# Optimization experiments

Hardware: AMD Instinct MI355X
Metric: run time of the kernel (lower is better)

## Reference

```python
import jax, jax.numpy as jnp
import numpy as np

N_NODES = 100000
N_EDGES = 3200000
D_IN = 256
D_OUT = 128
LN_EPS = 1e-5


def setup_inputs() -> dict:
    key = jax.random.key(0)
    ks = jax.random.split(key, 6)
    stdv = 1.0 / np.sqrt(D_OUT)
    x = jax.random.normal(ks[0], (N_NODES, D_IN), dtype=jnp.float32)
    weight = jax.random.uniform(ks[1], (D_IN, D_OUT), minval=-stdv, maxval=stdv, dtype=jnp.float32)
    bias = jnp.zeros((D_OUT,), dtype=jnp.float32)
    res_w = jax.random.normal(ks[2], (D_IN, D_OUT), dtype=jnp.float32) * 0.05
    res_b = jnp.zeros((D_OUT,), dtype=jnp.float32)
    ln_gamma = jnp.ones((D_OUT,), dtype=jnp.float32)
    ln_beta = jnp.zeros((D_OUT,), dtype=jnp.float32)
    edge_weight = jax.random.uniform(ks[3], (N_EDGES,), dtype=jnp.float32)
    edge_index = jax.random.randint(ks[4], (2, N_EDGES), 0, N_NODES, dtype=jnp.int32)
    return {"x": x, "weight": weight, "bias": bias, "res_w": res_w, "res_b": res_b,
            "ln_gamma": ln_gamma, "ln_beta": ln_beta,
            "edge_weight": edge_weight, "edge_index": edge_index}


def reference(x, weight, bias, res_w, res_b, ln_gamma, ln_beta, edge_weight, edge_index):
    # dense projection: [N, D_IN] @ [D_IN, D_OUT]
    support = x @ weight
    # spmm: out[dst] += w_e * support[src]  (weighted COO aggregation)
    src, dst = edge_index[0], edge_index[1]
    msg = support[src] * edge_weight[:, None]          # [E, D_OUT]
    out = jax.ops.segment_sum(msg, dst, num_segments=N_NODES)
    # fused bias + activated residual branch
    out = out + bias + jax.nn.relu(x @ res_w + res_b)
    # layernorm over feature dim
    mu = jnp.mean(out, axis=-1, keepdims=True)
    var = jnp.mean(jnp.square(out - mu), axis=-1, keepdims=True)
    out = (out - mu) * jax.lax.rsqrt(var + LN_EPS) * ln_gamma + ln_beta
    return out
```

## Files before the change

kernel.cpp:

```cpp
#include <hip/hip_runtime.h>
#include <hip/hip_bf16.h>

#define D_IN 256
#define D_OUT 128
#define LN_EPS 1e-5f
#define NBUCK 256
#define NCHUNK 256

typedef short bf16x8 __attribute__((ext_vector_type(8)));
typedef float f32x4 __attribute__((ext_vector_type(4)));
typedef unsigned short ushort_t;

__device__ __forceinline__ float b2f(ushort_t u) {
    union { unsigned int i; float f; } v; v.i = (unsigned int)u << 16; return v.f;
}
__device__ __forceinline__ ushort_t f2b(float f) {
    __hip_bfloat16 h = __float2bfloat16(f);
    return *reinterpret_cast<ushort_t*>(&h);
}

__global__ void k_transpose(const float* __restrict__ w, const float* __restrict__ rw,
                            ushort_t* __restrict__ wt) {
    int idx = blockIdx.x * 256 + threadIdx.x;
    int n = idx >> 8, k = idx & 255;
    float v = (n < 128) ? w[k * 128 + n] : rw[k * 128 + (n - 128)];
    wt[idx] = f2b(v);
}

__launch_bounds__(256)
__global__ void k_gemm(const float* __restrict__ x, const ushort_t* __restrict__ wt,
                       const float* __restrict__ bias, const float* __restrict__ res_b,
                       ushort_t* __restrict__ support, float* __restrict__ out, int n_nodes) {
    __shared__ ushort_t As[64 * 40];
    __shared__ ushort_t Bs[256 * 40];

    const int tid = threadIdx.x;
    const int m0 = blockIdx.x * 64;
    const int wv = tid >> 6, lane = tid & 63;
    const int lm = lane & 15, quad = lane >> 4;
    const int mh = wv >> 1;
    const int nh = wv & 1;

    f32x4 acc[2][8];
#pragma unroll
    for (int i = 0; i < 2; i++)
#pragma unroll
        for (int j = 0; j < 8; j++) acc[i][j] = 0.0f;

    const int arow = tid >> 2, aseg = tid & 3;
    const bool arow_ok = (m0 + arow) < n_nodes;
    const float* xrow = x + (long)(m0 + arow) * D_IN + aseg * 8;

    for (int kc = 0; kc < 8; kc++) {
        __syncthreads();
        {
            bf16x8 av = {0, 0, 0, 0, 0, 0, 0, 0};
            if (arow_ok) {
                f32x4 p0 = *(const f32x4*)(xrow + kc * 32);
                f32x4 p1 = *(const f32x4*)(xrow + kc * 32 + 4);
#pragma unroll
                for (int j = 0; j < 4; j++) { av[j] = (short)f2b(p0[j]); av[4 + j] = (short)f2b(p1[j]); }
            }
            *(bf16x8*)(&As[arow * 40 + aseg * 8]) = av;
        }
#pragma unroll
        for (int i = 0; i < 4; i++) {
            int n = (tid >> 2) + i * 64;
            bf16x8 v = *(const bf16x8*)(wt + n * 256 + kc * 32 + aseg * 8);
            *(bf16x8*)(&Bs[n * 40 + aseg * 8]) = v;
        }
        __syncthreads();

        bf16x8 afr0 = *(const bf16x8*)(&As[(mh * 32 + lm) * 40 + quad * 8]);
        bf16x8 afr1 = *(const bf16x8*)(&As[(mh * 32 + 16 + lm) * 40 + quad * 8]);
#pragma unroll
        for (int nt = 0; nt < 8; nt++) {
            bf16x8 bfr = *(const bf16x8*)(&Bs[(nh * 128 + nt * 16 + lm) * 40 + quad * 8]);
            acc[0][nt] = __builtin_amdgcn_mfma_f32_16x16x32_bf16(afr0, bfr, acc[0][nt], 0, 0, 0);
            acc[1][nt] = __builtin_amdgcn_mfma_f32_16x16x32_bf16(afr1, bfr, acc[1][nt], 0, 0, 0);
        }
    }

#pragma unroll
    for (int i = 0; i < 2; i++) {
#pragma unroll
        for (int nt = 0; nt < 8; nt++) {
            int col = nh * 128 + nt * 16 + lm;
#pragma unroll
            for (int r = 0; r < 4; r++) {
                int node = m0 + mh * 32 + i * 16 + quad * 4 + r;
                if (node >= n_nodes) continue;
                float v = acc[i][nt][r];
                if (col < 128) {
                    support[(long)node * 128 + col] = f2b(v);
                } else {
                    int c2 = col - 128;
                    float t = v + res_b[c2];
                    t = t > 0.0f ? t : 0.0f;
                    out[(long)node * 128 + c2] = t + bias[c2];
                }
            }
        }
    }
}

__launch_bounds__(256)
__global__ void k_count(const int* __restrict__ ei, int* __restrict__ cntmat, int E, int chunk) {
    __shared__ int h[NBUCK];
    int c = blockIdx.x, t = threadIdx.x;
    h[t] = 0;
    __syncthreads();
    int lo = c * chunk, hi = min(lo + chunk, E);
    for (int e = lo + t; e < hi; e += 256)
        atomicAdd(&h[(unsigned)ei[E + e] >> 9], 1);
    __syncthreads();
    cntmat[t * NCHUNK + c] = h[t];
}

__launch_bounds__(256)
__global__ void k_scan1(int* __restrict__ cntmat, int* __restrict__ rowsum) {
    __shared__ int sh[256];
    int b = blockIdx.x, t = threadIdx.x;
    int v = cntmat[b * NCHUNK + t];
    sh[t] = v;
    __syncthreads();
    for (int off = 1; off < 256; off <<= 1) {
        int x = sh[t]; int add = (t >= off) ? sh[t - off] : 0;
        __syncthreads(); sh[t] = x + add; __syncthreads();
    }
    cntmat[b * NCHUNK + t] = sh[t] - v;
    if (t == 255) rowsum[b] = sh[255];
}

__launch_bounds__(256)
__global__ void k_scan2(const int* __restrict__ rowsum, int* __restrict__ bucket_base,
                        int* __restrict__ offs, int n_nodes, int E) {
    __shared__ int sh[256];
    int t = threadIdx.x;
    int v = rowsum[t];
    sh[t] = v;
    __syncthreads();
    for (int off = 1; off < 256; off <<= 1) {
        int x = sh[t]; int add = (t >= off) ? sh[t - off] : 0;
        __syncthreads(); sh[t] = x + add; __syncthreads();
    }
    bucket_base[t] = sh[t] - v;
    if (t == 255) bucket_base[256] = sh[255];
    if (t == 0) offs[n_nodes] = E;
}

__launch_bounds__(256)
__global__ void k_part(const int* __restrict__ ei, const float* __restrict__ ew,
                       const int* __restrict__ cntmat, const int* __restrict__ bucket_base,
                       int2* __restrict__ srcw, int E, int chunk) {
    __shared__ int cur[NBUCK];
    int c = blockIdx.x, t = threadIdx.x;
    cur[t] = bucket_base[t] + cntmat[t * NCHUNK + c];
    __syncthreads();
    int lo = c * chunk, hi = min(lo + chunk, E);
    for (int e = lo + t; e < hi; e += 256) {
        int src = ei[e];
        int dst = ei[E + e];
        float w = ew[e];
        int b = (unsigned)dst >> 9;
        int pos = atomicAdd(&cur[b], 1);
        int2 rec;
        rec.x = src | ((dst & 511) << 17);
        rec.y = __float_as_int(w);
        srcw[pos] = rec;
    }
}

__launch_bounds__(256)
__global__ void k_build(const int2* __restrict__ srcw, const int* __restrict__ bucket_base,
                        int* __restrict__ perm, int* __restrict__ offs, int n_nodes) {
    __shared__ int h[512];
    __shared__ int psum[256];
    int b = blockIdx.x, t = threadIdx.x;
    int start = bucket_base[b], end = bucket_base[b + 1];
    h[t] = 0; h[t + 256] = 0;
    __syncthreads();
    for (int i = start + t; i < end; i += 256)
        atomicAdd(&h[(unsigned)srcw[i].x >> 17], 1);
    __syncthreads();
    int h0 = h[2 * t], h1 = h[2 * t + 1];
    int p = h0 + h1;
    psum[t] = p;
    __syncthreads();
    for (int off = 1; off < 256; off <<= 1) {
        int x = psum[t]; int add = (t >= off) ? psum[t - off] : 0;
        __syncthreads(); psum[t] = x + add; __syncthreads();
    }
    int e0 = psum[t] - p;
    int e1 = e0 + h0;
    h[2 * t] = e0; h[2 * t + 1] = e1;
    int node0 = b * 512 + 2 * t;
    if (node0 < n_nodes) offs[node0] = start + e0;
    if (node0 + 1 < n_nodes) offs[node0 + 1] = start + e1;
    __syncthreads();
    for (int i = start + t; i < end; i += 256) {
        int dl = (unsigned)srcw[i].x >> 17;
        int pos = start + atomicAdd(&h[dl], 1);
        perm[pos] = i;
    }
}

__launch_bounds__(256)
__global__ void k_agg_ln(const ushort_t* __restrict__ support, const int* __restrict__ offs,
                         const int* __restrict__ perm, const int2* __restrict__ srcw,
                         const float* __restrict__ gamma, const float* __restrict__ beta,
                         float* __restrict__ out, int n_nodes) {
    int gw = (int)((blockIdx.x * blockDim.x + threadIdx.x) >> 6);
    int lane = threadIdx.x & 63;
    int nw = (int)((gridDim.x * blockDim.x) >> 6);
    float g0 = gamma[lane * 2], g1 = gamma[lane * 2 + 1];
    float b0 = beta[lane * 2], b1 = beta[lane * 2 + 1];

    for (int node = gw; node < n_nodes; node += nw) {
        int start = offs[node], end = offs[node + 1];
        float ax = 0.0f, ay = 0.0f;
        for (int base = start; base < end; base += 64) {
            int n = end - base; if (n > 64) n = 64;
            int2 ed = {0, 0};
            if (lane < n) ed = srcw[perm[base + lane]];
            for (int j = 0; j < n; j++) {
                int srcj = __builtin_amdgcn_readlane(ed.x, j) & 131071;
                float wj = __int_as_float(__builtin_amdgcn_readlane(ed.y, j));
                unsigned int v = *(const unsigned int*)(support + (long)srcj * 128 + lane * 2);
                ax += wj * b2f((ushort_t)(v & 0xffffu));
                ay += wj * b2f((ushort_t)(v >> 16));
            }
        }
        float2 r = *(const float2*)(out + (long)node * 128 + lane * 2);
        float tx = ax + r.x, ty = ay + r.y;
        float s = tx + ty;
        float ss = tx * tx + ty * ty;
#pragma unroll
        for (int off = 1; off < 64; off <<= 1) {
            s += __shfl_xor(s, off, 64);
            ss += __shfl_xor(ss, off, 64);
        }
        float mean = s * (1.0f / 128.0f);
        float var = ss * (1.0f / 128.0f) - mean * mean;
        float rstd = rsqrtf(var + LN_EPS);
        float2 o;
        o.x = (tx - mean) * rstd * g0 + b0;
        o.y = (ty - mean) * rstd * g1 + b1;
        *(float2*)(out + (long)node * 128 + lane * 2) = o;
    }
}

extern "C" void kernel_launch(void* const* d_in, const int* in_sizes, int n_in,
                              void* d_out, int out_size, void* d_ws, size_t ws_size,
                              hipStream_t stream) {
    const float* x      = (const float*)d_in[0];
    const float* weight = (const float*)d_in[1];
    const float* bias   = (const float*)d_in[2];
    const float* res_w  = (const float*)d_in[3];
    const float* res_b  = (const float*)d_in[4];
    const float* gamma  = (const float*)d_in[5];
    const float* beta   = (const float*)d_in[6];
    const float* ew     = (const float*)d_in[7];
    const int*   ei     = (const int*)d_in[8];

    const int E = in_sizes[7];
    const int n_nodes = in_sizes[0] / D_IN;
    const int chunk = (E + NCHUNK - 1) / NCHUNK;
    float* out = (float*)d_out;

    char* ws = (char*)d_ws;
    size_t off = 0;
    auto alloc = [&](size_t bytes) { void* p = ws + off; off = (off + bytes + 255) & ~(size_t)255; return p; };
    ushort_t* wt      = (ushort_t*)alloc(256 * 256 * 2);
    ushort_t* support = (ushort_t*)alloc((size_t)n_nodes * 128 * 2);
    int* cntmat       = (int*)alloc((size_t)NBUCK * NCHUNK * 4);
    int* rowsum       = (int*)alloc(NBUCK * 4);
    int* bucket_base  = (int*)alloc((NBUCK + 1) * 4);
    int* offs         = (int*)alloc((size_t)(n_nodes + 1) * 4);
    int2* srcw        = (int2*)alloc((size_t)E * 8);
    int* perm         = (int*)alloc((size_t)E * 4);

    k_transpose<<<256, 256, 0, stream>>>(weight, res_w, wt);
    k_gemm<<<(n_nodes + 63) / 64, 256, 0, stream>>>(x, wt, bias, res_b, support, out, n_nodes);
    k_count<<<NCHUNK, 256, 0, stream>>>(ei, cntmat, E, chunk);
    k_scan1<<<NBUCK, 256, 0, stream>>>(cntmat, rowsum);
    k_scan2<<<1, 256, 0, stream>>>(rowsum, bucket_base, offs, n_nodes, E);
    k_part<<<NCHUNK, 256, 0, stream>>>(ei, ew, cntmat, bucket_base, srcw, E, chunk);
    k_build<<<NBUCK, 256, 0, stream>>>(srcw, bucket_base, perm, offs, n_nodes);
    k_agg_ln<<<4096, 256, 0, stream>>>(support, offs, perm, srcw, gamma, beta, out, n_nodes);
}
```

Before: 538.0 us.

## Materialize sorted edge arrays with bf16 weights and unroll gather loop

The partition stage now writes separate key and bf16 weight arrays, and the build stage writes fully sorted key/weight arrays instead of a permutation index. The aggregation kernel therefore reads edges contiguously rather than through a perm indirection. Its inner gather loop is also unrolled by four so several support loads are in flight at once. Storing edge weights in bf16 loses precision, and the build stage now does extra scattered writes.

```diff
diff --git a/kernel.cpp b/kernel.cpp
--- a/kernel.cpp
+++ b/kernel.cpp
@@ -152,7 +152,7 @@
 __launch_bounds__(256)
 __global__ void k_part(const int* __restrict__ ei, const float* __restrict__ ew,
                        const int* __restrict__ cntmat, const int* __restrict__ bucket_base,
-                       int2* __restrict__ srcw, int E, int chunk) {
+                       int* __restrict__ pk, ushort_t* __restrict__ pw, int E, int chunk) {
     __shared__ int cur[NBUCK];
     int c = blockIdx.x, t = threadIdx.x;
     cur[t] = bucket_base[t] + cntmat[t * NCHUNK + c];
@@ -164,16 +164,15 @@
         float w = ew[e];
         int b = (unsigned)dst >> 9;
         int pos = atomicAdd(&cur[b], 1);
-        int2 rec;
-        rec.x = src | ((dst & 511) << 17);
-        rec.y = __float_as_int(w);
-        srcw[pos] = rec;
-    }
-}
-
-__launch_bounds__(256)
-__global__ void k_build(const int2* __restrict__ srcw, const int* __restrict__ bucket_base,
-                        int* __restrict__ perm, int* __restrict__ offs, int n_nodes) {
+        pk[pos] = src | ((dst & 511) << 17);
+        pw[pos] = f2b(w);
+    }
+}
+
+__launch_bounds__(256)
+__global__ void k_build(const int* __restrict__ pk, const ushort_t* __restrict__ pw,
+                        const int* __restrict__ bucket_base, int* __restrict__ sk,
+                        ushort_t* __restrict__ sw, int* __restrict__ offs, int n_nodes) {
     __shared__ int h[512];
     __shared__ int psum[256];
     int b = blockIdx.x, t = threadIdx.x;
@@ -181,7 +180,7 @@
     h[t] = 0; h[t + 256] = 0;
     __syncthreads();
     for (int i = start + t; i < end; i += 256)
-        atomicAdd(&h[(unsigned)srcw[i].x >> 17], 1);
+        atomicAdd(&h[(unsigned)pk[i] >> 17], 1);
     __syncthreads();
     int h0 = h[2 * t], h1 = h[2 * t + 1];
     int p = h0 + h1;
@@ -199,15 +198,17 @@
     if (node0 + 1 < n_nodes) offs[node0 + 1] = start + e1;
     __syncthreads();
     for (int i = start + t; i < end; i += 256) {
-        int dl = (unsigned)srcw[i].x >> 17;
+        int key = pk[i];
+        int dl = (unsigned)key >> 17;
         int pos = start + atomicAdd(&h[dl], 1);
-        perm[pos] = i;
+        sk[pos] = key;
+        sw[pos] = pw[i];
     }
 }
 
 __launch_bounds__(256)
 __global__ void k_agg_ln(const ushort_t* __restrict__ support, const int* __restrict__ offs,
-                         const int* __restrict__ perm, const int2* __restrict__ srcw,
+                         const int* __restrict__ sk, const ushort_t* __restrict__ sw,
                          const float* __restrict__ gamma, const float* __restrict__ beta,
                          float* __restrict__ out, int n_nodes) {
     int gw = (int)((blockIdx.x * blockDim.x + threadIdx.x) >> 6);
@@ -221,12 +222,34 @@
         float ax = 0.0f, ay = 0.0f;
         for (int base = start; base < end; base += 64) {
             int n = end - base; if (n > 64) n = 64;
-            int2 ed = {0, 0};
-            if (lane < n) ed = srcw[perm[base + lane]];
-            for (int j = 0; j < n; j++) {
-                int srcj = __builtin_amdgcn_readlane(ed.x, j) & 131071;
-                float wj = __int_as_float(__builtin_amdgcn_readlane(ed.y, j));
-                unsigned int v = *(const unsigned int*)(support + (long)srcj * 128 + lane * 2);
+            int key = 0, wbits = 0;
+            if (lane < n) {
+                key = sk[base + lane];
+                wbits = (int)sw[base + lane];
+            }
+            int j = 0;
+            for (; j + 4 <= n; j += 4) {
+                int s0 = __builtin_amdgcn_readlane(key, j + 0) & 131071;
+                int s1 = __builtin_amdgcn_readlane(key, j + 1) & 131071;
+                int s2 = __builtin_amdgcn_readlane(key, j + 2) & 131071;
+                int s3 = __builtin_amdgcn_readlane(key, j + 3) & 131071;
+                float w0 = b2f((ushort_t)__builtin_amdgcn_readlane(wbits, j + 0));
+                float w1 = b2f((ushort_t)__builtin_amdgcn_readlane(wbits, j + 1));
+                float w2 = b2f((ushort_t)__builtin_amdgcn_readlane(wbits, j + 2));
+                float w3 = b2f((ushort_t)__builtin_amdgcn_readlane(wbits, j + 3));
+                unsigned int v0 = *(const unsigned int*)(support + (long)s0 * 128 + lane * 2);
+                unsigned int v1 = *(const unsigned int*)(support + (long)s1 * 128 + lane * 2);
+                unsigned int v2 = *(const unsigned int*)(support + (long)s2 * 128 + lane * 2);
+                unsigned int v3 = *(const unsigned int*)(support + (long)s3 * 128 + lane * 2);
+                ax += w0 * b2f((ushort_t)(v0 & 0xffffu)) + w1 * b2f((ushort_t)(v1 & 0xffffu))
+                    + w2 * b2f((ushort_t)(v2 & 0xffffu)) + w3 * b2f((ushort_t)(v3 & 0xffffu));
+                ay += w0 * b2f((ushort_t)(v0 >> 16)) + w1 * b2f((ushort_t)(v1 >> 16))
+                    + w2 * b2f((ushort_t)(v2 >> 16)) + w3 * b2f((ushort_t)(v3 >> 16));
+            }
+            for (; j < n; j++) {
+                int sj = __builtin_amdgcn_readlane(key, j) & 131071;
+                float wj = b2f((ushort_t)__builtin_amdgcn_readlane(wbits, j));
+                unsigned int v = *(const unsigned int*)(support + (long)sj * 128 + lane * 2);
                 ax += wj * b2f((ushort_t)(v & 0xffffu));
                 ay += wj * b2f((ushort_t)(v >> 16));
             }
@@ -277,15 +300,17 @@
     int* rowsum       = (int*)alloc(NBUCK * 4);
     int* bucket_base  = (int*)alloc((NBUCK + 1) * 4);
     int* offs         = (int*)alloc((size_t)(n_nodes + 1) * 4);
-    int2* srcw        = (int2*)alloc((size_t)E * 8);
-    int* perm         = (int*)alloc((size_t)E * 4);
+    int* pk           = (int*)alloc((size_t)E * 4);
+    ushort_t* pw      = (ushort_t*)alloc((size_t)E * 2);
+    int* sk           = (int*)alloc((size_t)E * 4);
+    ushort_t* sw      = (ushort_t*)alloc((size_t)E * 2);
 
     k_transpose<<<256, 256, 0, stream>>>(weight, res_w, wt);
     k_gemm<<<(n_nodes + 63) / 64, 256, 0, stream>>>(x, wt, bias, res_b, support, out, n_nodes);
     k_count<<<NCHUNK, 256, 0, stream>>>(ei, cntmat, E, chunk);
     k_scan1<<<NBUCK, 256, 0, stream>>>(cntmat, rowsum);
     k_scan2<<<1, 256, 0, stream>>>(rowsum, bucket_base, offs, n_nodes, E);
-    k_part<<<NCHUNK, 256, 0, stream>>>(ei, ew, cntmat, bucket_base, srcw, E, chunk);
-    k_build<<<NBUCK, 256, 0, stream>>>(srcw, bucket_base, perm, offs, n_nodes);
-    k_agg_ln<<<4096, 256, 0, stream>>>(support, offs, perm, srcw, gamma, beta, out, n_nodes);
-}
+    k_part<<<NCHUNK, 256, 0, stream>>>(ei, ew, cntmat, bucket_base, pk, pw, E, chunk);
+    k_build<<<NBUCK, 256, 0, stream>>>(pk, pw, bucket_base, sk, sw, offs, n_nodes);
+    k_agg_ln<<<4096, 256, 0, stream>>>(support, offs, sk, sw, gamma, beta, out, n_nodes);
+}
```

Result: faster. 505.1 us (-6.1%).
